# Kernel optimization log

Hardware: AMD Instinct MI355X
Metric: run time of the kernel (lower is better)

Reference implementation:

```python
import jax, jax.numpy as jnp
import numpy as np

B = 16384
D_IN = 1024
D_OUT = 512
H1 = 4 * D_IN      # floor(layersDimentions[0]*inputDimention) = 4096
H3 = 4 * D_OUT     # floor(layersDimentions[1]*outputDimention) = 2048
H4 = 4 * D_OUT     # floor(layersDimentions[2]*outputDimention) = 2048
M = 256            # codebook size


def _linear_params(key, fan_in, fan_out):
    kw, kb = jax.random.split(key)
    bound = 1.0 / np.sqrt(fan_in)
    w = jax.random.uniform(kw, (fan_out, fan_in), jnp.float32, -bound, bound)
    b = jax.random.uniform(kb, (fan_out,), jnp.float32, -bound, bound)
    return w, b


def setup_inputs() -> dict:
    key = jax.random.key(0)
    ks = jax.random.split(key, 7)
    x = jax.random.normal(ks[0], (B, D_IN), jnp.float32)
    codebook = jnp.sort(jax.random.normal(ks[1], (M,), jnp.float32))
    w1, b1 = _linear_params(ks[2], D_IN, H1)
    w2, b2 = _linear_params(ks[3], H1, D_OUT)
    w3, b3 = _linear_params(ks[4], D_OUT, H3)
    w4, b4 = _linear_params(ks[5], H3, H4)
    w5, b5 = _linear_params(ks[6], H4, D_OUT)
    return {"x": x, "codebook": codebook,
            "w1": w1, "b1": b1, "w2": w2, "b2": b2,
            "w3": w3, "b3": b3, "w4": w4, "b4": b4,
            "w5": w5, "b5": b5}


def _quantize(x, codebook):
    # nearest codeword per scalar element: argmin_m |x - c_m|
    # x: [B, D], codebook: [M]
    d = jnp.abs(x[..., None] - codebook)          # [B, D, M]
    idx = jnp.argmin(d, axis=-1)                  # [B, D]
    return codebook[idx]


def reference(x, codebook, w1, b1, w2, b2, w3, b3, w4, b4, w5, b5):
    h = x @ w1.T + b1                # [B, H1]
    h = h @ w2.T + b2                # [B, D_OUT]
    h = _quantize(h, codebook)       # [B, D_OUT]
    h = h @ w3.T + b3                # [B, H3]
    h = h @ w4.T + b4                # [B, H4]
    return h @ w5.T + b5             # [B, D_OUT]
```

## Files before the change

### kernel.cpp

```cpp
#include <hip/hip_runtime.h>


typedef __bf16 v8bf __attribute__((ext_vector_type(8)));
typedef float  v4f  __attribute__((ext_vector_type(4)));

#define Bdim   16384
#define DIN    1024
#define DOUT   512
#define H1dim  4096
#define H3dim  2048
#define H4dim  2048

#define GLOBAL_AS __attribute__((address_space(1)))
#define LDS_AS    __attribute__((address_space(3)))

__device__ __forceinline__ void load16_to_lds(const __bf16* g, __bf16* l) {
  __builtin_amdgcn_global_load_lds((const GLOBAL_AS unsigned int*)g,
                                   (LDS_AS unsigned int*)l, 16, 0, 0);
}

__device__ __forceinline__ unsigned pack2bf(float a, float b) {
  return (unsigned)__builtin_bit_cast(unsigned short, (__bf16)a) |
         ((unsigned)__builtin_bit_cast(unsigned short, (__bf16)b) << 16);
}

__device__ __forceinline__ void transpose_body(const float* __restrict__ in,
                                               __bf16* __restrict__ out,
                                               int R, int C, int bx, int by,
                                               float (*tile)[68]) {
  const int c0 = bx * 32, r0 = by * 64;
  const int t = threadIdx.x, tr = t >> 5, tc = t & 31;
#pragma unroll
  for (int i = 0; i < 8; ++i)
    tile[tc][tr + i * 8] = in[(size_t)(r0 + tr + i * 8) * C + (c0 + tc)];
  __syncthreads();
  const int orow = t >> 3, oc = (t & 7) * 8;
  float4 a = *(const float4*)&tile[orow][oc];
  float4 b = *(const float4*)&tile[orow][oc + 4];
  int4 o;
  o.x = pack2bf(a.x, a.y); o.y = pack2bf(a.z, a.w);
  o.z = pack2bf(b.x, b.y); o.w = pack2bf(b.z, b.w);
  *(int4*)&out[(size_t)(c0 + orow) * R + (r0 + oc)] = o;
}

__device__ __forceinline__ void cast_body(const float* __restrict__ in,
                                          __bf16* __restrict__ out, int b) {
  const size_t i = (size_t)b * 2048 + (size_t)threadIdx.x * 8;
  float4 a = *(const float4*)&in[i];
  float4 c = *(const float4*)&in[i + 4];
  int4 o;
  o.x = pack2bf(a.x, a.y); o.y = pack2bf(a.z, a.w);
  o.z = pack2bf(c.x, c.y); o.w = pack2bf(c.z, c.w);
  *(int4*)&out[i] = o;
}

__global__ void prep_kernel(const float* __restrict__ w1, __bf16* __restrict__ w1T,
                            const float* __restrict__ w4, __bf16* __restrict__ w4T,
                            const float* __restrict__ w3, __bf16* __restrict__ w3T,
                            const float* __restrict__ x, __bf16* __restrict__ xb,
                            const float* __restrict__ w2, __bf16* __restrict__ w2b,
                            const float* __restrict__ w5, __bf16* __restrict__ w5b) {
  __shared__ float tile[32][68];
  int b = blockIdx.x;
  if (b < 2048) {
    transpose_body(w1, w1T, H1dim, DIN, b & 31, b >> 5, tile);
  } else if (b < 4096) {
    b -= 2048;
    transpose_body(w4, w4T, H4dim, H3dim, b & 63, b >> 6, tile);
  } else if (b < 4608) {
    b -= 4096;
    transpose_body(w3, w3T, H3dim, DOUT, b & 15, b >> 4, tile);
  } else if (b < 12800) {
    cast_body(x, xb, b - 4608);
  } else if (b < 13824) {
    cast_body(w2, w2b, b - 12800);
  } else {
    cast_body(w5, w5b, b - 13824);
  }
}

__device__ __forceinline__ void bias_ba_body(int bb, const float* __restrict__ b1,
                                             const float* __restrict__ w2,
                                             const float* __restrict__ b2,
                                             float* __restrict__ ba) {
  const int wave = threadIdx.x >> 6, lane = threadIdx.x & 63;
  const int j = bb * 4 + wave;
  float s = 0.f;
  for (int k = lane; k < H1dim; k += 64) s += b1[k] * w2[(size_t)j * H1dim + k];
#pragma unroll
  for (int off = 32; off; off >>= 1) s += __shfl_xor(s, off, 64);
  if (lane == 0) ba[j] = s + b2[j];
}

__device__ __forceinline__ void bias_bc_body(int bb, const float* __restrict__ b3,
                                             const __bf16* __restrict__ WtT,
                                             const float* __restrict__ b4,
                                             const float* __restrict__ w5,
                                             const float* __restrict__ b5,
                                             float* __restrict__ bc) {
  const int wave = threadIdx.x >> 6, lane = threadIdx.x & 63;
  const int j = bb * 4 + wave;
  float s = 0.f;
  for (int k = lane; k < H4dim; k += 64)
    s += b3[k] * (float)WtT[(size_t)j * H4dim + k] + b4[k] * w5[(size_t)j * H4dim + k];
#pragma unroll
  for (int off = 32; off; off >>= 1) s += __shfl_xor(s, off, 64);
  if (lane == 0) bc[j] = s + b5[j];
}

#define ASM_BAR() asm volatile("s_barrier" ::: "memory")

__device__ __forceinline__ void fold_body(__bf16* As, __bf16* Bs,
                                          int bx, int by,
                                          const __bf16* __restrict__ A,
                                          const __bf16* __restrict__ Bt,
                                          __bf16* __restrict__ Cout,
                                          int M, int N, int K, int CH) {
  const int t = threadIdx.x;
  const int m0 = bx * 64, n0 = by * 64;
  const int lane = t & 63, wave = t >> 6;
  const int quad = lane >> 4, l15 = lane & 15;
  const int wm = (wave & 1) * 32, wn = (wave >> 1) * 32;

  const int lrow = lane >> 3;
  const int gcol = ((lane & 7) ^ lrow) * 8;
  const __bf16* gA = A  + (size_t)(m0 + 16 * wave + lrow) * K + gcol;
  const __bf16* gB = Bt + (size_t)(n0 + 16 * wave + lrow) * K + gcol;
  const int swz = l15 & 7;

  v4f acc[2][2], accT[2][2];
#pragma unroll
  for (int i = 0; i < 2; ++i)
#pragma unroll
    for (int j = 0; j < 2; ++j) {
      acc[i][j] = (v4f){0.f, 0.f, 0.f, 0.f};
      accT[i][j] = (v4f){0.f, 0.f, 0.f, 0.f};
    }

  auto stage = [&](int k0, int buf) {
    __bf16* lA = As + buf * 4096 + 16 * wave * 64;
    __bf16* lB = Bs + buf * 4096 + 16 * wave * 64;
#pragma unroll
    for (int p = 0; p < 2; ++p)
      load16_to_lds(gA + (size_t)(8 * p) * K + k0, lA + p * 512);
#pragma unroll
    for (int p = 0; p < 2; ++p)
      load16_to_lds(gB + (size_t)(8 * p) * K + k0, lB + p * 512);
  };

  const int nk = K >> 6;
  const int chsteps = CH >> 6;
  stage(0, 0);
  stage(64, 1);

  int cc = 0;
  for (int tk = 0; tk < nk; ++tk) {
    if (tk + 1 < nk) asm volatile("s_waitcnt vmcnt(4)" ::: "memory");
    else             asm volatile("s_waitcnt vmcnt(0)" ::: "memory");
    ASM_BAR();

    const __bf16* cA = As + (tk & 1) * 4096;
    const __bf16* cB = Bs + (tk & 1) * 4096;
#pragma unroll
    for (int kk = 0; kk < 2; ++kk) {
      const int cch = ((kk * 4 + quad) ^ swz) * 8;
      v8bf af[2], bv[2];
#pragma unroll
      for (int i = 0; i < 2; ++i)
        af[i] = *(const v8bf*)&cA[(wm + i * 16 + l15) * 64 + cch];
#pragma unroll
      for (int j = 0; j < 2; ++j)
        bv[j] = *(const v8bf*)&cB[(wn + j * 16 + l15) * 64 + cch];
#pragma unroll
      for (int i = 0; i < 2; ++i)
#pragma unroll
        for (int j = 0; j < 2; ++j)
          acc[i][j] = __builtin_amdgcn_mfma_f32_16x16x32_bf16(af[i], bv[j], acc[i][j], 0, 0, 0);
    }
    if (++cc == chsteps) {
      cc = 0;
#pragma unroll
      for (int i = 0; i < 2; ++i)
#pragma unroll
        for (int j = 0; j < 2; ++j) {
          accT[i][j] += acc[i][j];
          acc[i][j] = (v4f){0.f, 0.f, 0.f, 0.f};
        }
    }
    asm volatile("s_waitcnt lgkmcnt(0)" ::: "memory");
    ASM_BAR();
    if (tk + 2 < nk) stage((tk + 2) << 6, tk & 1);
  }

#pragma unroll
  for (int j = 0; j < 2; ++j) {
    const int gn = n0 + wn + j * 16 + l15;
#pragma unroll
    for (int i = 0; i < 2; ++i)
#pragma unroll
      for (int r2 = 0; r2 < 4; ++r2) {
        const int gm = m0 + wm + i * 16 + quad * 4 + r2;
        Cout[(size_t)gm * N + gn] = (__bf16)accT[i][j][r2];
      }
  }
}

enum { MODE_Q = 1, MODE_OUT = 2 };

template <int MODE>
__device__ __forceinline__ void gemm128_body(__bf16* As, __bf16* Bs, float* cbs,
                                             int bx, int by,
                                             const __bf16* __restrict__ A,
                                             const __bf16* __restrict__ Bt,
                                             void* __restrict__ Cout,
                                             const float* __restrict__ bias,
                                             const float* __restrict__ codebook,
                                             int M, int N, int K) {
  const int t = threadIdx.x;
  const int m0 = bx * 128, n0 = by * 128;
  if constexpr (MODE == MODE_Q) cbs[t] = codebook[t];

  const int lane = t & 63, wave = t >> 6;
  const int quad = lane >> 4, l15 = lane & 15;
  const int wm = (wave & 1) * 64, wn = (wave >> 1) * 64;

  const int lrow = lane >> 3;
  const int gcol = ((lane & 7) ^ lrow) * 8;
  const __bf16* gA = A  + (size_t)(m0 + 32 * wave + lrow) * K + gcol;
  const __bf16* gB = Bt + (size_t)(n0 + 32 * wave + lrow) * K + gcol;
  const int swz = l15 & 7;

  v4f acc[4][4];
#pragma unroll
  for (int i = 0; i < 4; ++i)
#pragma unroll
    for (int j = 0; j < 4; ++j) acc[i][j] = (v4f){0.f, 0.f, 0.f, 0.f};

  auto stage = [&](int k0, int buf) {
    __bf16* lA = As + buf * 8192 + 32 * wave * 64;
    __bf16* lB = Bs + buf * 8192 + 32 * wave * 64;
#pragma unroll
    for (int p = 0; p < 4; ++p)
      load16_to_lds(gA + (size_t)(8 * p) * K + k0, lA + p * 512);
#pragma unroll
    for (int p = 0; p < 4; ++p)
      load16_to_lds(gB + (size_t)(8 * p) * K + k0, lB + p * 512);
  };

  const int nk = K >> 6;
  stage(0, 0);
  stage(64, 1);

  for (int tk = 0; tk < nk; ++tk) {
    if (tk + 1 < nk) asm volatile("s_waitcnt vmcnt(8)" ::: "memory");
    else             asm volatile("s_waitcnt vmcnt(0)" ::: "memory");
    ASM_BAR();

    const __bf16* cA = As + (tk & 1) * 8192;
    const __bf16* cB = Bs + (tk & 1) * 8192;
#pragma unroll
    for (int kk = 0; kk < 2; ++kk) {
      const int cch = ((kk * 4 + quad) ^ swz) * 8;
      v8bf af[4], bv[4];
#pragma unroll
      for (int i = 0; i < 4; ++i)
        af[i] = *(const v8bf*)&cA[(wm + i * 16 + l15) * 64 + cch];
#pragma unroll
      for (int j = 0; j < 4; ++j)
        bv[j] = *(const v8bf*)&cB[(wn + j * 16 + l15) * 64 + cch];
#pragma unroll
      for (int i = 0; i < 4; ++i)
#pragma unroll
        for (int j = 0; j < 4; ++j)
          acc[i][j] = __builtin_amdgcn_mfma_f32_16x16x32_bf16(af[i], bv[j], acc[i][j], 0, 0, 0);
    }
    asm volatile("s_waitcnt lgkmcnt(0)" ::: "memory");
    ASM_BAR();
    if (tk + 2 < nk) stage((tk + 2) << 6, tk & 1);
  }

#pragma unroll
  for (int j = 0; j < 4; ++j) {
    const int gn = n0 + wn + j * 16 + l15;
    const float bj = bias[gn];
#pragma unroll
    for (int i = 0; i < 4; ++i) {
#pragma unroll
      for (int r = 0; r < 4; ++r) {
        const int gm = m0 + wm + i * 16 + quad * 4 + r;
        float v = acc[i][j][r] + bj;
        if constexpr (MODE == MODE_Q) {
          int idx = 0;
#pragma unroll
          for (int s = 128; s > 0; s >>= 1) {
            const int u = idx + s;
            if (cbs[u] <= v) idx = u;
          }
          float best = cbs[idx];
          if (idx < 255) {
            const float c1 = cbs[idx + 1];
            if (!(v - best <= c1 - v)) best = c1;
          }
          ((__bf16*)Cout)[(size_t)gm * N + gn] = (__bf16)best;
        } else {
          ((float*)Cout)[(size_t)gm * N + gn] = v;
        }
      }
    }
  }
}

__global__ __launch_bounds__(256, 3)
void foldA_kernel(const __bf16* __restrict__ w2b, const __bf16* __restrict__ w1T,
                  __bf16* __restrict__ WaT,
                  const __bf16* __restrict__ w5b, const __bf16* __restrict__ w4T,
                  __bf16* __restrict__ WtT,
                  const float* __restrict__ b1, const float* __restrict__ w2,
                  const float* __restrict__ b2, float* __restrict__ ba) {
  __shared__ __align__(16) __bf16 As[2 * 64 * 64];
  __shared__ __align__(16) __bf16 Bs[2 * 64 * 64];
  int b = blockIdx.x;
  if (b < 128) {
    const int c = b & 7, i = b >> 3;
    fold_body(As, Bs, i >> 1, c * 2 + (i & 1), w2b, w1T, WaT,
              DOUT, DIN, H1dim, 512);
  } else if (b < 384) {
    b -= 128;
    const int c = b & 7, i = b >> 3;
    fold_body(As, Bs, i >> 2, c * 4 + (i & 3), w5b, w4T, WtT,
              DOUT, H3dim, H4dim, 512);
  } else {
    bias_ba_body(b - 384, b1, w2, b2, ba);
  }
}

__global__ __launch_bounds__(256, 2)
void foldB_kernel(const __bf16* __restrict__ WtT, const __bf16* __restrict__ w3T,
                  __bf16* __restrict__ WcT,
                  const float* __restrict__ b3, const float* __restrict__ b4,
                  const float* __restrict__ w5, const float* __restrict__ b5,
                  float* __restrict__ bc,
                  const __bf16* __restrict__ xb, const __bf16* __restrict__ WaT,
                  __bf16* __restrict__ q, const float* __restrict__ ba,
                  const float* __restrict__ cb) {
  __shared__ __align__(16) __bf16 As[2 * 128 * 64];
  __shared__ __align__(16) __bf16 Bs[2 * 128 * 64];
  __shared__ float cbs[256];
  int b = blockIdx.x;
  if (b < 64) {
    const int c = b & 7, i = b >> 3;
    fold_body(As, Bs, i, c, WtT, w3T, WcT, DOUT, DOUT, H3dim, 256);
  } else if (b < 192) {
    bias_bc_body(b - 64, b3, WtT, b4, w5, b5, bc);
  } else {
    b -= 192;
    const int c = b & 7, i = b >> 3;
    gemm128_body<MODE_Q>(As, Bs, cbs, c * 16 + (i >> 2), i & 3, xb, WaT, q,
                         ba, cb, Bdim, DOUT, DIN);
  }
}

__global__ __launch_bounds__(256, 2)
void gemmout_kernel(const __bf16* __restrict__ q, const __bf16* __restrict__ WcT,
                    float* __restrict__ out, const float* __restrict__ bc) {
  __shared__ __align__(16) __bf16 As[2 * 128 * 64];
  __shared__ __align__(16) __bf16 Bs[2 * 128 * 64];
  const int b = blockIdx.x;
  const int c = b & 7, i = b >> 3;
  gemm128_body<MODE_OUT>(As, Bs, nullptr, c * 16 + (i >> 2), i & 3,
                         q, WcT, out, bc, nullptr, Bdim, DOUT, DOUT);
}

extern "C" void kernel_launch(void* const* d_in, const int* in_sizes, int n_in,
                              void* d_out, int out_size, void* d_ws, size_t ws_size,
                              hipStream_t stream) {
  const float* x  = (const float*)d_in[0];
  const float* cb = (const float*)d_in[1];
  const float* w1 = (const float*)d_in[2];
  const float* b1 = (const float*)d_in[3];
  const float* w2 = (const float*)d_in[4];
  const float* b2 = (const float*)d_in[5];
  const float* w3 = (const float*)d_in[6];
  const float* b3 = (const float*)d_in[7];
  const float* w4 = (const float*)d_in[8];
  const float* b4 = (const float*)d_in[9];
  const float* w5 = (const float*)d_in[10];
  const float* b5 = (const float*)d_in[11];
  float* out = (float*)d_out;

  char* ws = (char*)d_ws;
  size_t off = 0;
  auto alloc = [&](size_t bytes) -> void* {
    void* p = ws + off;
    off = (off + bytes + 255) & ~(size_t)255;
    return p;
  };
  __bf16* w1T = (__bf16*)alloc((size_t)DIN * H1dim * 2);
  __bf16* w4T = (__bf16*)alloc((size_t)H3dim * H4dim * 2);
  __bf16* w3T = (__bf16*)alloc((size_t)DOUT * H3dim * 2);
  __bf16* w2b = (__bf16*)alloc((size_t)DOUT * H1dim * 2);
  __bf16* w5b = (__bf16*)alloc((size_t)DOUT * H4dim * 2);
  __bf16* WaT = (__bf16*)alloc((size_t)DOUT * DIN * 2);
  __bf16* WtT = (__bf16*)alloc((size_t)DOUT * H3dim * 2);
  __bf16* WcT = (__bf16*)alloc((size_t)DOUT * DOUT * 2);
  __bf16* q   = (__bf16*)alloc((size_t)Bdim * DOUT * 2);
  __bf16* xb  = (__bf16*)alloc((size_t)Bdim * DIN * 2);
  float*  ba  = (float*)alloc(DOUT * 4);
  float*  bc  = (float*)alloc(DOUT * 4);

  prep_kernel<<<14336, 256, 0, stream>>>(w1, w1T, w4, w4T, w3, w3T,
                                         x, xb, w2, w2b, w5, w5b);

  foldA_kernel<<<512, 256, 0, stream>>>(w2b, w1T, WaT, w5b, w4T, WtT,
                                        b1, w2, b2, ba);

  foldB_kernel<<<704, 256, 0, stream>>>(WtT, w3T, WcT, b3, b4, w5, b5, bc,
                                        xb, WaT, q, ba, cb);

  gemmout_kernel<<<512, 256, 0, stream>>>(q, WcT, out, bc);
}
```

Measured before the change: 273.7 us.

## Use 128x64 GEMM tiles with register-staged A and higher occupancy

```diff
diff --git a/kernel.cpp b/kernel.cpp
--- a/kernel.cpp
+++ b/kernel.cpp
@@ -43,15 +43,20 @@
   *(int4*)&out[(size_t)(c0 + orow) * R + (r0 + oc)] = o;
 }
 
-__device__ __forceinline__ void cast_body(const float* __restrict__ in,
-                                          __bf16* __restrict__ out, int b) {
-  const size_t i = (size_t)b * 2048 + (size_t)threadIdx.x * 8;
-  float4 a = *(const float4*)&in[i];
-  float4 c = *(const float4*)&in[i + 4];
-  int4 o;
-  o.x = pack2bf(a.x, a.y); o.y = pack2bf(a.z, a.w);
-  o.z = pack2bf(c.x, c.y); o.w = pack2bf(c.z, c.w);
-  *(int4*)&out[i] = o;
+__device__ __forceinline__ void cast16_body(const float* __restrict__ in,
+                                            __bf16* __restrict__ out, int b) {
+  const size_t i = (size_t)b * 4096 + (size_t)threadIdx.x * 16;
+  float4 a0 = *(const float4*)&in[i];
+  float4 a1 = *(const float4*)&in[i + 4];
+  float4 a2 = *(const float4*)&in[i + 8];
+  float4 a3 = *(const float4*)&in[i + 12];
+  int4 o0, o1;
+  o0.x = pack2bf(a0.x, a0.y); o0.y = pack2bf(a0.z, a0.w);
+  o0.z = pack2bf(a1.x, a1.y); o0.w = pack2bf(a1.z, a1.w);
+  o1.x = pack2bf(a2.x, a2.y); o1.y = pack2bf(a2.z, a2.w);
+  o1.z = pack2bf(a3.x, a3.y); o1.w = pack2bf(a3.z, a3.w);
+  *(int4*)&out[i] = o0;
+  *(int4*)&out[i + 8] = o1;
 }
 
 __global__ void prep_kernel(const float* __restrict__ w1, __bf16* __restrict__ w1T,
@@ -70,12 +75,12 @@
   } else if (b < 4608) {
     b -= 4096;
     transpose_body(w3, w3T, H3dim, DOUT, b & 15, b >> 4, tile);
-  } else if (b < 12800) {
-    cast_body(x, xb, b - 4608);
-  } else if (b < 13824) {
-    cast_body(w2, w2b, b - 12800);
+  } else if (b < 8704) {
+    cast16_body(x, xb, b - 4608);
+  } else if (b < 9216) {
+    cast16_body(w2, w2b, b - 8704);
   } else {
-    cast_body(w5, w5b, b - 13824);
+    cast16_body(w5, w5b, b - 9216);
   }
 }
 
@@ -208,79 +213,105 @@
 enum { MODE_Q = 1, MODE_OUT = 2 };
 
 template <int MODE>
-__device__ __forceinline__ void gemm128_body(__bf16* As, __bf16* Bs, float* cbs,
-                                             int bx, int by,
-                                             const __bf16* __restrict__ A,
-                                             const __bf16* __restrict__ Bt,
-                                             void* __restrict__ Cout,
-                                             const float* __restrict__ bias,
-                                             const float* __restrict__ codebook,
-                                             int M, int N, int K) {
+__device__ __forceinline__ void gemmr_body(__bf16* As, __bf16* Bs, float* cbs,
+                                           int bx, int by,
+                                           const __bf16* __restrict__ A,
+                                           const __bf16* __restrict__ Bt,
+                                           void* __restrict__ Cout,
+                                           const float* __restrict__ bias,
+                                           const float* __restrict__ codebook,
+                                           int M, int N, int K) {
   const int t = threadIdx.x;
-  const int m0 = bx * 128, n0 = by * 128;
+  const int m0 = bx * 128, n0 = by * 64;
   if constexpr (MODE == MODE_Q) cbs[t] = codebook[t];
 
   const int lane = t & 63, wave = t >> 6;
   const int quad = lane >> 4, l15 = lane & 15;
-  const int wm = (wave & 1) * 64, wn = (wave >> 1) * 64;
-
-  const int lrow = lane >> 3;
-  const int gcol = ((lane & 7) ^ lrow) * 8;
-  const __bf16* gA = A  + (size_t)(m0 + 32 * wave + lrow) * K + gcol;
-  const __bf16* gB = Bt + (size_t)(n0 + 32 * wave + lrow) * K + gcol;
+  const int wm = (wave & 1) * 64, wn = (wave >> 1) * 32;
   const int swz = l15 & 7;
 
-  v4f acc[4][4];
-#pragma unroll
-  for (int i = 0; i < 4; ++i)
-#pragma unroll
-    for (int j = 0; j < 4; ++j) acc[i][j] = (v4f){0.f, 0.f, 0.f, 0.f};
-
-  auto stage = [&](int k0, int buf) {
-    __bf16* lA = As + buf * 8192 + 32 * wave * 64;
-    __bf16* lB = Bs + buf * 8192 + 32 * wave * 64;
-#pragma unroll
-    for (int p = 0; p < 4; ++p)
-      load16_to_lds(gA + (size_t)(8 * p) * K + k0, lA + p * 512);
-#pragma unroll
-    for (int p = 0; p < 4; ++p)
+  const int r0 = lane >> 3, ca = lane & 7;
+  const __bf16* gA = A + (size_t)(m0 + 32 * wave + r0) * K + ca * 8;
+  const int awr = (32 * wave + r0) * 64 + ((ca ^ r0) * 8);
+
+  const int gcolB = ((lane & 7) ^ r0) * 8;
+  const __bf16* gB = Bt + (size_t)(n0 + 16 * wave + r0) * K + gcolB;
+
+  auto stageB = [&](int k0, int buf) {
+    __bf16* lB = Bs + buf * 4096 + 16 * wave * 64;
+#pragma unroll
+    for (int p = 0; p < 2; ++p)
       load16_to_lds(gB + (size_t)(8 * p) * K + k0, lB + p * 512);
   };
 
+  v4f acc[4][2];
+#pragma unroll
+  for (int i = 0; i < 4; ++i)
+#pragma unroll
+    for (int j = 0; j < 2; ++j) acc[i][j] = (v4f){0.f, 0.f, 0.f, 0.f};
+
   const int nk = K >> 6;
-  stage(0, 0);
-  stage(64, 1);
-
-  for (int tk = 0; tk < nk; ++tk) {
-    if (tk + 1 < nk) asm volatile("s_waitcnt vmcnt(8)" ::: "memory");
-    else             asm volatile("s_waitcnt vmcnt(0)" ::: "memory");
-    ASM_BAR();
-
-    const __bf16* cA = As + (tk & 1) * 8192;
-    const __bf16* cB = Bs + (tk & 1) * 8192;
+  int4 ra0[4], ra1[4];
+
+#pragma unroll
+  for (int p = 0; p < 4; ++p) ra0[p] = *(const int4*)(gA + (size_t)(8 * p) * K);
+#pragma unroll
+  for (int p = 0; p < 4; ++p) ra1[p] = *(const int4*)(gA + (size_t)(8 * p) * K + 64);
+  stageB(0, 0);
+  stageB(64, 1);
+  asm volatile("s_waitcnt vmcnt(8)" ::: "memory");
+#pragma unroll
+  for (int p = 0; p < 4; ++p) *(int4*)&As[awr + p * 512] = ra0[p];
+  asm volatile("s_waitcnt vmcnt(2)" ::: "memory");
+  asm volatile("s_waitcnt lgkmcnt(0)" ::: "memory");
+  ASM_BAR();
+
+  auto step = [&](int tk, int4 (&rcur)[4], int4 (&rnext)[4]) {
+    if (tk + 2 < nk) {
+#pragma unroll
+      for (int p = 0; p < 4; ++p)
+        rcur[p] = *(const int4*)(gA + (size_t)(8 * p) * K + (tk + 2) * 64);
+    }
+    const __bf16* cB = Bs + (tk & 1) * 4096;
 #pragma unroll
     for (int kk = 0; kk < 2; ++kk) {
       const int cch = ((kk * 4 + quad) ^ swz) * 8;
-      v8bf af[4], bv[4];
+      v8bf af[4], bv[2];
 #pragma unroll
       for (int i = 0; i < 4; ++i)
-        af[i] = *(const v8bf*)&cA[(wm + i * 16 + l15) * 64 + cch];
-#pragma unroll
-      for (int j = 0; j < 4; ++j)
+        af[i] = *(const v8bf*)&As[(wm + i * 16 + l15) * 64 + cch];
+#pragma unroll
+      for (int j = 0; j < 2; ++j)
         bv[j] = *(const v8bf*)&cB[(wn + j * 16 + l15) * 64 + cch];
 #pragma unroll
       for (int i = 0; i < 4; ++i)
 #pragma unroll
-        for (int j = 0; j < 4; ++j)
+        for (int j = 0; j < 2; ++j)
           acc[i][j] = __builtin_amdgcn_mfma_f32_16x16x32_bf16(af[i], bv[j], acc[i][j], 0, 0, 0);
     }
     asm volatile("s_waitcnt lgkmcnt(0)" ::: "memory");
     ASM_BAR();
-    if (tk + 2 < nk) stage((tk + 2) << 6, tk & 1);
-  }
-
-#pragma unroll
-  for (int j = 0; j < 4; ++j) {
+    if (tk + 2 < nk) {
+      stageB((tk + 2) << 6, tk & 1);
+      asm volatile("s_waitcnt vmcnt(6)" ::: "memory");
+    } else {
+      asm volatile("s_waitcnt vmcnt(0)" ::: "memory");
+    }
+    if (tk + 1 < nk) {
+#pragma unroll
+      for (int p = 0; p < 4; ++p) *(int4*)&As[awr + p * 512] = rnext[p];
+      asm volatile("s_waitcnt lgkmcnt(0)" ::: "memory");
+      ASM_BAR();
+    }
+  };
+
+  for (int tk = 0; tk < nk; tk += 2) {
+    step(tk, ra0, ra1);
+    step(tk + 1, ra1, ra0);
+  }
+
+#pragma unroll
+  for (int j = 0; j < 2; ++j) {
     const int gn = n0 + wn + j * 16 + l15;
     const float bj = bias[gn];
 #pragma unroll
@@ -334,7 +365,7 @@
   }
 }
 
-__global__ __launch_bounds__(256, 2)
+__global__ __launch_bounds__(256, 4)
 void foldB_kernel(const __bf16* __restrict__ WtT, const __bf16* __restrict__ w3T,
                   __bf16* __restrict__ WcT,
                   const float* __restrict__ b3, const float* __restrict__ b4,
@@ -343,8 +374,8 @@
                   const __bf16* __restrict__ xb, const __bf16* __restrict__ WaT,
                   __bf16* __restrict__ q, const float* __restrict__ ba,
                   const float* __restrict__ cb) {
-  __shared__ __align__(16) __bf16 As[2 * 128 * 64];
-  __shared__ __align__(16) __bf16 Bs[2 * 128 * 64];
+  __shared__ __align__(16) __bf16 As[128 * 64];
+  __shared__ __align__(16) __bf16 Bs[2 * 64 * 64];
   __shared__ float cbs[256];
   int b = blockIdx.x;
   if (b < 64) {
@@ -355,20 +386,20 @@
   } else {
     b -= 192;
     const int c = b & 7, i = b >> 3;
-    gemm128_body<MODE_Q>(As, Bs, cbs, c * 16 + (i >> 2), i & 3, xb, WaT, q,
-                         ba, cb, Bdim, DOUT, DIN);
-  }
-}
-
-__global__ __launch_bounds__(256, 2)
+    gemmr_body<MODE_Q>(As, Bs, cbs, c * 16 + (i >> 3), i & 7, xb, WaT, q,
+                       ba, cb, Bdim, DOUT, DIN);
+  }
+}
+
+__global__ __launch_bounds__(256, 4)
 void gemmout_kernel(const __bf16* __restrict__ q, const __bf16* __restrict__ WcT,
                     float* __restrict__ out, const float* __restrict__ bc) {
-  __shared__ __align__(16) __bf16 As[2 * 128 * 64];
-  __shared__ __align__(16) __bf16 Bs[2 * 128 * 64];
+  __shared__ __align__(16) __bf16 As[128 * 64];
+  __shared__ __align__(16) __bf16 Bs[2 * 64 * 64];
   const int b = blockIdx.x;
   const int c = b & 7, i = b >> 3;
-  gemm128_body<MODE_OUT>(As, Bs, nullptr, c * 16 + (i >> 2), i & 3,
-                         q, WcT, out, bc, nullptr, Bdim, DOUT, DOUT);
+  gemmr_body<MODE_OUT>(As, Bs, nullptr, c * 16 + (i >> 3), i & 7,
+                       q, WcT, out, bc, nullptr, Bdim, DOUT, DOUT);
 }
 
 extern "C" void kernel_launch(void* const* d_in, const int* in_sizes, int n_in,
@@ -408,14 +439,14 @@
   float*  ba  = (float*)alloc(DOUT * 4);
   float*  bc  = (float*)alloc(DOUT * 4);
 
-  prep_kernel<<<14336, 256, 0, stream>>>(w1, w1T, w4, w4T, w3, w3T,
-                                         x, xb, w2, w2b, w5, w5b);
+  prep_kernel<<<9472, 256, 0, stream>>>(w1, w1T, w4, w4T, w3, w3T,
+                                        x, xb, w2, w2b, w5, w5b);
 
   foldA_kernel<<<512, 256, 0, stream>>>(w2b, w1T, WaT, w5b, w4T, WtT,
                                         b1, w2, b2, ba);
 
-  foldB_kernel<<<704, 256, 0, stream>>>(WtT, w3T, WcT, b3, b4, w5, b5, bc,
-                                        xb, WaT, q, ba, cb);
-
-  gemmout_kernel<<<512, 256, 0, stream>>>(q, WcT, out, bc);
-}
+  foldB_kernel<<<1216, 256, 0, stream>>>(WtT, w3T, WcT, b3, b4, w5, b5, bc,
+                                         xb, WaT, q, ba, cb);
+
+  gemmout_kernel<<<1024, 256, 0, stream>>>(q, WcT, out, bc);
+}
```

Result: slower. 340.8 us (+24.5%).
